# Optimization experiments

Measured on AMD Instinct MI355X. Metric: run time of the kernel, lower is better.

## Reference

```python
import jax, jax.numpy as jnp
import numpy as np

N_STATE, N_CTRL, T, NB = 32, 16, 128, 64
NSC = N_STATE + N_CTRL

mT = lambda m: jnp.swapaxes(m, -1, -2)


def setup_inputs() -> dict:
    key = jax.random.key(0)
    k1, k2, k3, k4, k5, k6 = jax.random.split(key, 6)
    # Q must be PSD (the torch example builds Q = Qr^T Qr); add I for conditioning.
    Qr = jax.random.normal(k1, (NB, T, NSC, NSC), jnp.float32)
    Q = mT(Qr) @ Qr / NSC + jnp.eye(NSC, dtype=jnp.float32)
    p = jax.random.normal(k2, (NB, T, NSC), jnp.float32)
    x_init = jax.random.normal(k3, (NB, N_STATE), jnp.float32)
    # Stable-ish linear dynamics so the T=128 rollout does not blow up.
    A = jnp.tile(0.95 * jnp.eye(N_STATE, dtype=jnp.float32), (NB, 1, 1)) \
        + 0.02 * jax.random.normal(k4, (NB, N_STATE, N_STATE), jnp.float32)
    Bm = 0.1 * jax.random.normal(k5, (NB, N_STATE, N_CTRL), jnp.float32)
    c1 = 0.1 * jax.random.normal(k6, (NB, N_STATE), jnp.float32)
    return {"x_init": x_init, "Q": Q, "p": p, "A": A, "Bm": Bm, "c1": c1}


def _gains(Qt, qt, ns):
    # Qt: [B, nsc, nsc], qt: [B, nsc, 1]
    Qxx, Qxu = Qt[:, :ns, :ns], Qt[:, :ns, ns:]
    Qux, Quu = Qt[:, ns:, :ns], Qt[:, ns:, ns:]
    qx, qu = qt[:, :ns], qt[:, ns:]
    Quu_inv = jnp.linalg.pinv(Quu)          # batched pinv, as in the torch code
    K = -(Quu_inv @ Qux)                    # [B, nc, ns]
    k = -(Quu_inv @ qu)                     # [B, nc, 1]
    KT = mT(K)
    V = Qxx + Qxu @ K + KT @ Qux + KT @ Quu @ K
    v = qx + Qxu @ k + KT @ qu + KT @ Quu @ k
    return K, k, V, v


def _lqr(x_init, Q, p, A, Bm, c1):
    ns = A.shape[-1]
    F = jnp.concatenate([A, Bm], axis=-1)   # [B, ns, nsc]
    FT = mT(F)
    ft = c1[..., None]                       # [B, ns, 1]

    # ---- backward Riccati/DP recursion (sequential over T) ----
    K_last, k_last, V, v = _gains(Q[:, -1], p[:, -1][..., None], ns)

    def bstep(carry, inp):
        Vtp1, vtp1 = carry
        Qt_raw, pt = inp                     # [B,nsc,nsc], [B,nsc]
        Qt = Qt_raw + FT @ Vtp1 @ F
        qt = pt[..., None] + FT @ (Vtp1 @ ft) + FT @ vtp1
        K, k, Vt, vt = _gains(Qt, qt, ns)
        return (Vt, vt), (K, k)

    Qtm = jnp.swapaxes(Q[:, :-1], 0, 1)[::-1]   # [T-1, B, nsc, nsc], t = T-2..0
    ptm = jnp.swapaxes(p[:, :-1], 0, 1)[::-1]
    _, (Ks_rev, ks_rev) = jax.lax.scan(bstep, (V, v), (Qtm, ptm))
    Ks = jnp.concatenate([Ks_rev[::-1], K_last[None]], axis=0)  # [T, B, nc, ns], forward time order
    ks = jnp.concatenate([ks_rev[::-1], k_last[None]], axis=0)  # [T, B, nc, 1]

    # ---- forward rollout ----
    def fstep(x, inp):
        K, k, Qt, pt = inp
        u = jnp.einsum('bij,bj->bi', K, x) + k[..., 0]
        xu = jnp.concatenate([x, u], axis=-1)                 # tau_t, [B, nsc]
        obj = 0.5 * jnp.einsum('bi,bij,bj->b', xu, Qt, xu) + jnp.einsum('bi,bi->b', xu, pt)
        xn = jnp.einsum('bij,bj->bi', A, x) + jnp.einsum('bij,bj->bi', Bm, u) + c1
        return xn, (x, u, obj, xu)

    Qf = jnp.swapaxes(Q, 0, 1)               # [T, B, nsc, nsc]
    pf = jnp.swapaxes(p, 0, 1)
    _, (xs, us, objs, taus) = jax.lax.scan(fstep, x_init, (Ks, ks, Qf, pf))
    # xs: [T, B, ns] (x_0..x_{T-1}, matching torch which does not append x_T)
    return xs, us, objs, taus


def reference(x_init, Q, p, A, Bm, c1):
    return _lqr(x_init, Q, p, A, Bm, c1)
```

## Files before the change

### kernel.cpp

```cpp
#include <hip/hip_runtime.h>

#define TT     128
#define NBATCH 64

#define BAR()  asm volatile("s_waitcnt lgkmcnt(0)\n\ts_barrier" ::: "memory")
#define BARV() asm volatile("s_waitcnt vmcnt(0) lgkmcnt(0)\n\ts_barrier" ::: "memory")

__device__ __forceinline__ void gload16(const float* g, float* l) {
    __builtin_amdgcn_global_load_lds(
        (__attribute__((address_space(1))) void*)g,
        (__attribute__((address_space(3))) void*)l, 16, 0, 0);
}

__device__ __forceinline__ float rdlane(float v, int l) {
    return __int_as_float(__builtin_amdgcn_readlane(__float_as_int(v), l));
}

__device__ __forceinline__ void inv4(const float4 pr[4], float IP[4][4]) {
    float a00=pr[0].x, a01=pr[0].y, a10=pr[1].x, a11=pr[1].y;
    float b00=pr[0].z, b01=pr[0].w, b10=pr[1].z, b11=pr[1].w;
    float c00=pr[2].x, c01=pr[2].y, c10=pr[3].x, c11=pr[3].y;
    float d00=pr[2].z, d01=pr[2].w, d10=pr[3].z, d11=pr[3].w;
    float r = 1.0f / (a00*a11 - a01*a10);
    float ia00 =  a11*r, ia01 = -a01*r, ia10 = -a10*r, ia11 = a00*r;
    float t00 = ia00*b00 + ia01*b10, t01 = ia00*b01 + ia01*b11;
    float t10 = ia10*b00 + ia11*b10, t11 = ia10*b01 + ia11*b11;
    float u00 = c00*ia00 + c01*ia10, u01 = c00*ia01 + c01*ia11;
    float u10 = c10*ia00 + c11*ia10, u11 = c10*ia01 + c11*ia11;
    float s00 = d00 - (c00*t00 + c01*t10), s01 = d01 - (c00*t01 + c01*t11);
    float s10 = d10 - (c10*t00 + c11*t10), s11 = d11 - (c10*t01 + c11*t11);
    float rs = 1.0f / (s00*s11 - s01*s10);
    float is00 =  s11*rs, is01 = -s01*rs, is10 = -s10*rs, is11 = s00*rs;
    float su00 = is00*u00 + is01*u10, su01 = is00*u01 + is01*u11;
    float su10 = is10*u00 + is11*u10, su11 = is10*u01 + is11*u11;
    IP[0][0] = ia00 + (t00*su00 + t01*su10);
    IP[0][1] = ia01 + (t00*su01 + t01*su11);
    IP[1][0] = ia10 + (t10*su00 + t11*su10);
    IP[1][1] = ia11 + (t10*su01 + t11*su11);
    IP[0][2] = -(t00*is00 + t01*is10);  IP[0][3] = -(t00*is01 + t01*is11);
    IP[1][2] = -(t10*is00 + t11*is10);  IP[1][3] = -(t10*is01 + t11*is11);
    IP[2][0] = -su00; IP[2][1] = -su01;
    IP[3][0] = -su10; IP[3][1] = -su11;
    IP[2][2] = is00;  IP[2][3] = is01;
    IP[3][2] = is10;  IP[3][3] = is11;
}

__global__ __launch_bounds__(256, 1)
void lqr_backward(const float* __restrict__ Q, const float* __restrict__ p,
                  const float* __restrict__ A, const float* __restrict__ Bm,
                  const float* __restrict__ c1, float* __restrict__ Kws)
{
    const int b   = blockIdx.x;
    const int tid = threadIdx.x;

    __shared__ __align__(16) float Fs[32*52];
    __shared__ __align__(16) float Vs[32*36];
    __shared__ __align__(16) float Ms[32*52];
    __shared__ __align__(16) float Xs[48*52];
    __shared__ __align__(16) float Qtb[2][48*48];
    __shared__ __align__(16) float qtb[2][256];
    __shared__ __align__(16) float KKs[16*36];
    __shared__ float vsv[32], fts[32], wv[32];

    const int ai0 = (tid / 12) * 4, ac0 = (tid % 12) * 4;
    const int br0 = (tid / 12) * 4, bc0 = (tid % 12) * 4;
    const int pi  = tid >> 3;
    const int pg  = tid & 7;
    const int pj0 = pg * 4;

    for (int st = tid; st < 256; st += 256) {
        int k = st >> 3, q = st & 7;
        ((float4*)(Fs + k*52))[q] = ((const float4*)A)[(b*32 + k)*8 + q];
    }
    for (int st = tid; st < 128; st += 256) {
        int k = st >> 2, q = st & 3;
        ((float4*)(Fs + k*52))[8 + q] = ((const float4*)Bm)[(b*32 + k)*4 + q];
    }
    for (int st = tid; st < 288; st += 256) ((float4*)Vs)[st] = make_float4(0,0,0,0);
    if (tid < 32) { vsv[tid] = 0.0f; fts[tid] = c1[b*32 + tid]; }

    {
        const float* Qs0 = Q + (size_t)(b*TT + TT-1) * 2304;
        #pragma unroll
        for (int r = 0; r < 3; ++r) {
            int e = r*256 + tid;
            if (e < 576) gload16(Qs0 + e*4, Qtb[0] + e*4);
        }
        if (tid < 12) gload16(p + (size_t)(b*TT + TT-1)*48 + tid*4, qtb[0] + tid*4);
    }
    BARV();

    for (int t = TT-1; t >= 0; --t) {
        const int cur = (TT-1 - t) & 1;
        float* Qtc = Qtb[cur];
        float* qtc = qtb[cur];
        float* Kbase = Kws + (size_t)(b*TT + t) * 528;

        if (tid < 96) {
            float4 a0 = make_float4(0,0,0,0), a1 = a0, a2 = a0, a3 = a0;
            #pragma unroll
            for (int k = 0; k < 32; ++k) {
                float4 v = *(const float4*)(Vs + k*36 + ai0);
                float4 f = *(const float4*)(Fs + k*52 + ac0);
                a0.x += v.x*f.x; a0.y += v.x*f.y; a0.z += v.x*f.z; a0.w += v.x*f.w;
                a1.x += v.y*f.x; a1.y += v.y*f.y; a1.z += v.y*f.z; a1.w += v.y*f.w;
                a2.x += v.z*f.x; a2.y += v.z*f.y; a2.z += v.z*f.z; a2.w += v.z*f.w;
                a3.x += v.w*f.x; a3.y += v.w*f.y; a3.z += v.w*f.z; a3.w += v.w*f.w;
            }
            *(float4*)(Ms + (ai0+0)*52 + ac0) = a0;
            *(float4*)(Ms + (ai0+1)*52 + ac0) = a1;
            *(float4*)(Ms + (ai0+2)*52 + ac0) = a2;
            *(float4*)(Ms + (ai0+3)*52 + ac0) = a3;
        } else if (tid >= 192) {
            const int idx = tid - 192;
            if (t > 0) {
                const float* Qs = Q + (size_t)(b*TT + t-1) * 2304;
                float* dst = Qtb[cur ^ 1];
                #pragma unroll
                for (int r = 0; r < 9; ++r) {
                    int e = r*64 + idx;
                    gload16(Qs + e*4, dst + e*4);
                }
                if (idx < 12) gload16(p + (size_t)(b*TT + t-1)*48 + idx*4,
                                      qtb[cur ^ 1] + idx*4);
            }
            if (idx < 32) {
                float acc = vsv[idx];
                #pragma unroll
                for (int k = 0; k < 32; ++k) acc += Vs[idx*36 + k] * fts[k];
                wv[idx] = acc;
            }
        }
        if (tid >= 192) {
            if (t > 0) asm volatile("s_waitcnt vmcnt(10)" ::: "memory");
            else       asm volatile("s_waitcnt vmcnt(0)"  ::: "memory");
        }
        BAR();

        if (tid < 144) {
            float4 a0 = *(const float4*)(Qtc + (br0+0)*48 + bc0);
            float4 a1 = *(const float4*)(Qtc + (br0+1)*48 + bc0);
            float4 a2 = *(const float4*)(Qtc + (br0+2)*48 + bc0);
            float4 a3 = *(const float4*)(Qtc + (br0+3)*48 + bc0);
            #pragma unroll
            for (int k = 0; k < 32; ++k) {
                float4 fr = *(const float4*)(Fs + k*52 + br0);
                float4 mc = *(const float4*)(Ms + k*52 + bc0);
                a0.x += fr.x*mc.x; a0.y += fr.x*mc.y; a0.z += fr.x*mc.z; a0.w += fr.x*mc.w;
                a1.x += fr.y*mc.x; a1.y += fr.y*mc.y; a1.z += fr.y*mc.z; a1.w += fr.y*mc.w;
                a2.x += fr.z*mc.x; a2.y += fr.z*mc.y; a2.z += fr.z*mc.z; a2.w += fr.z*mc.w;
                a3.x += fr.w*mc.x; a3.y += fr.w*mc.y; a3.z += fr.w*mc.z; a3.w += fr.w*mc.w;
            }
            *(float4*)(Xs + (br0+0)*52 + bc0) = a0;
            *(float4*)(Xs + (br0+1)*52 + bc0) = a1;
            *(float4*)(Xs + (br0+2)*52 + bc0) = a2;
            *(float4*)(Xs + (br0+3)*52 + bc0) = a3;
        } else if (tid >= 192 && tid < 240) {
            const int c = tid - 192;
            float acc = qtc[c];
            #pragma unroll
            for (int k = 0; k < 32; ++k) acc += Fs[k*52 + c] * wv[k];
            qtc[c] = acc;
            if (c >= 32) Xs[c*52 + 48] = acc;
        }
        BAR();

        float4 pa0; float pq[16];
        if (tid < 64) {
            const int c = (tid < 49) ? tid : 48;
            float col[16];
            #pragma unroll
            for (int r = 0; r < 16; ++r) col[r] = Xs[(32+r)*52 + c];

            #pragma unroll
            for (int q = 0; q < 4; ++q) {
                const int pc = 32 + 4*q;
                float4 pr[4];
                #pragma unroll
                for (int m = 0; m < 4; ++m) {
                    pr[m].x = rdlane(col[4*q+m], pc+0);
                    pr[m].y = rdlane(col[4*q+m], pc+1);
                    pr[m].z = rdlane(col[4*q+m], pc+2);
                    pr[m].w = rdlane(col[4*q+m], pc+3);
                }
                float IP[4][4];
                inv4(pr, IP);
                float R[4];
                #pragma unroll
                for (int m = 0; m < 4; ++m)
                    R[m] = IP[m][0]*col[4*q+0] + IP[m][1]*col[4*q+1]
                         + IP[m][2]*col[4*q+2] + IP[m][3]*col[4*q+3];
                #pragma unroll
                for (int r = 0; r < 16; ++r) {
                    if ((r >> 2) == q) continue;
                    float f0 = rdlane(col[r], pc+0);
                    float f1 = rdlane(col[r], pc+1);
                    float f2 = rdlane(col[r], pc+2);
                    float f3 = rdlane(col[r], pc+3);
                    col[r] -= f0*R[0] + f1*R[1] + f2*R[2] + f3*R[3];
                }
                #pragma unroll
                for (int m = 0; m < 4; ++m) col[4*q+m] = R[m];
            }

            const int cc = (tid < 32) ? c : 32;
            if (tid < 32 || tid == 48) {
                #pragma unroll
                for (int r = 0; r < 16; ++r) KKs[r*36 + cc] = col[r];
            }
        } else {
            pa0 = *(const float4*)(Xs + pi*52 + pj0);
            #pragma unroll
            for (int m = 0; m < 4; ++m) {
                float4 v4 = *(const float4*)(Xs + pi*52 + 32 + m*4);
                pq[m*4+0] = v4.x; pq[m*4+1] = v4.y;
                pq[m*4+2] = v4.z; pq[m*4+3] = v4.w;
            }
        }
        BAR();

        {
            if (tid < 64) {
                pa0 = *(const float4*)(Xs + pi*52 + pj0);
                #pragma unroll
                for (int m = 0; m < 4; ++m) {
                    float4 v4 = *(const float4*)(Xs + pi*52 + 32 + m*4);
                    pq[m*4+0] = v4.x; pq[m*4+1] = v4.y;
                    pq[m*4+2] = v4.z; pq[m*4+3] = v4.w;
                }
            }
            if (tid < 132) {
                const int ft = tid * 4;
                float4 kv;
                if (ft < 512) {
                    const int c = ft >> 4, r0 = ft & 15;
                    kv.x = -KKs[(r0+0)*36 + c];
                    kv.y = -KKs[(r0+1)*36 + c];
                    kv.z = -KKs[(r0+2)*36 + c];
                    kv.w = -KKs[(r0+3)*36 + c];
                } else {
                    const int r0 = ft - 512;
                    kv.x = -KKs[(r0+0)*36 + 32];
                    kv.y = -KKs[(r0+1)*36 + 32];
                    kv.z = -KKs[(r0+2)*36 + 32];
                    kv.w = -KKs[(r0+3)*36 + 32];
                }
                *(float4*)(Kbase + ft) = kv;
            }
            #pragma unroll
            for (int k = 0; k < 16; ++k) {
                float4 k0 = *(const float4*)(KKs + k*36 + pj0);
                pa0.x -= pq[k]*k0.x; pa0.y -= pq[k]*k0.y;
                pa0.z -= pq[k]*k0.z; pa0.w -= pq[k]*k0.w;
            }
            *(float4*)(Vs + pi*36 + pj0) = pa0;
            if (pg == 0) {
                float accv = qtc[pi];
                #pragma unroll
                for (int k = 0; k < 16; ++k) accv -= pq[k] * KKs[k*36 + 32];
                vsv[pi] = accv;
            }
        }
        BAR();
    }
}

__global__ __launch_bounds__(64, 1)
void lqr_forward(const float* __restrict__ Kws, const float* __restrict__ A,
                 const float* __restrict__ Bm, const float* __restrict__ c1,
                 const float* __restrict__ x_init,
                 float* __restrict__ xs, float* __restrict__ us,
                 float* __restrict__ taus)
{
    const int b = blockIdx.x, l = threadIdx.x;
    __shared__ __align__(16) float Fb[32*48];
    __shared__ __align__(16) float Kb[544];
    __shared__ float c1s[32], xu[48];

    for (int st = l; st < 256; st += 64) {
        int k = st >> 3, q = st & 7;
        ((float4*)Fb)[k*12 + q] = ((const float4*)A)[(b*32 + k)*8 + q];
    }
    for (int st = l; st < 128; st += 64) {
        int k = st >> 2, q = st & 3;
        ((float4*)Fb)[k*12 + 8 + q] = ((const float4*)Bm)[(b*32 + k)*4 + q];
    }
    if (l < 32) { c1s[l] = c1[b*32 + l]; xu[l] = x_init[b*32 + l]; }

    float4 ka, kb, kc = make_float4(0,0,0,0);
    {
        const float4* s0 = (const float4*)(Kws + (size_t)(b*TT) * 528);
        ka = s0[l]; kb = s0[l + 64];
        if (l < 4) kc = s0[l + 128];
    }
    __syncthreads();

    for (int t = 0; t < TT; ++t) {
        ((float4*)Kb)[l]      = ka;
        ((float4*)Kb)[l + 64] = kb;
        if (l < 4) ((float4*)Kb)[l + 128] = kc;
        __syncthreads();

        if (t + 1 < TT) {
            const float4* sn = (const float4*)(Kws + (size_t)(b*TT + t+1) * 528);
            ka = sn[l]; kb = sn[l + 64];
            if (l < 4) kc = sn[l + 128];
        }

        float part = 0.0f;
        int i = l & 15, g = l >> 4;
        #pragma unroll
        for (int jj = 0; jj < 8; ++jj) {
            int j = g*8 + jj;
            part += Kb[j*16 + i] * xu[j];
        }
        part += __shfl_down(part, 32);
        part += __shfl_down(part, 16);
        float ui = part + Kb[512 + i];
        if (l < 16) {
            xu[32 + l] = ui;
            us[(size_t)(t*64 + b)*16 + l] = ui;
        }
        __syncthreads();

        if (l < 32) xs[(size_t)(t*64 + b)*32 + l] = xu[l];
        if (l < 48) taus[(size_t)(t*64 + b)*48 + l] = xu[l];

        float pn = 0.0f;
        int i2 = l & 31, h = l >> 5;
        #pragma unroll
        for (int jj = 0; jj < 24; ++jj) {
            int j = h*24 + jj;
            pn += Fb[i2*48 + j] * xu[j];
        }
        pn += __shfl_down(pn, 32);
        float xni = pn + ((l < 32) ? c1s[i2] : 0.0f);
        __syncthreads();
        if (l < 32) xu[l] = xni;
        __syncthreads();
    }
}

__global__ __launch_bounds__(256, 4)
void lqr_obj(const float* __restrict__ Q, const float* __restrict__ p,
             const float* __restrict__ taus, float* __restrict__ objs)
{
    const int bi = blockIdx.x;
    const int b = bi >> 7, t = bi & 127;
    const int tid = threadIdx.x;
    __shared__ float xu[48];
    __shared__ float red[8];
    const float* tp = taus + (size_t)(t*64 + b)*48;
    if (tid < 48) xu[tid] = tp[tid];
    __syncthreads();

    const float4* Q4 = (const float4*)(Q + (size_t)bi * 2304);
    float acc = 0.0f;
    for (int e4 = tid; e4 < 576; e4 += 256) {
        float4 qv = Q4[e4];
        int r = e4 / 12, c = (e4 % 12) * 4;
        float xr = xu[r];
        acc += xr * (qv.x*xu[c] + qv.y*xu[c+1] + qv.z*xu[c+2] + qv.w*xu[c+3]);
    }
    acc *= 0.5f;
    if (tid < 48) acc += xu[tid] * p[(size_t)bi*48 + tid];

    #pragma unroll
    for (int off = 32; off > 0; off >>= 1) acc += __shfl_down(acc, off);
    if ((tid & 63) == 0) red[tid >> 6] = acc;
    __syncthreads();
    if (tid == 0) objs[(t << 6) + b] = red[0] + red[1] + red[2] + red[3];
}

extern "C" void kernel_launch(void* const* d_in, const int* in_sizes, int n_in,
                              void* d_out, int out_size, void* d_ws, size_t ws_size,
                              hipStream_t stream) {
    const float* x_init = (const float*)d_in[0];
    const float* Q      = (const float*)d_in[1];
    const float* p      = (const float*)d_in[2];
    const float* A      = (const float*)d_in[3];
    const float* Bm     = (const float*)d_in[4];
    const float* c1     = (const float*)d_in[5];

    float* out  = (float*)d_out;
    float* xs   = out;
    float* us   = out + 262144;
    float* objs = out + 393216;
    float* taus = out + 401408;

    float* Kws = (float*)d_ws;

    lqr_backward<<<NBATCH, 256, 0, stream>>>(Q, p, A, Bm, c1, Kws);
    lqr_forward<<<NBATCH, 64, 0, stream>>>(Kws, A, Bm, c1, x_init, xs, us, taus);
    lqr_obj<<<NBATCH*TT, 256, 0, stream>>>(Q, p, taus, objs);
}
```

Measured before the change: 689.0 us.

## Fuse Quu block update into solver wavefront and drop a barrier

After: 714.1 us. 3.6% more time.

```diff
diff --git a/kernel.cpp b/kernel.cpp
--- a/kernel.cpp
+++ b/kernel.cpp
@@ -63,7 +63,9 @@
     __shared__ float vsv[32], fts[32], wv[32];
 
     const int ai0 = (tid / 12) * 4, ac0 = (tid % 12) * 4;
-    const int br0 = (tid / 12) * 4, bc0 = (tid % 12) * 4;
+    const int ur0 = 32 + (tid / 12) * 4, uc0 = ac0;
+    const int xt  = tid - 64;
+    const int xr0 = (xt / 12) * 4, xc0 = (xt % 12) * 4;
     const int pi  = tid >> 3;
     const int pg  = tid & 7;
     const int pj0 = pg * 4;
@@ -137,36 +139,35 @@
         }
         BAR();
 
-        if (tid < 144) {
-            float4 a0 = *(const float4*)(Qtc + (br0+0)*48 + bc0);
-            float4 a1 = *(const float4*)(Qtc + (br0+1)*48 + bc0);
-            float4 a2 = *(const float4*)(Qtc + (br0+2)*48 + bc0);
-            float4 a3 = *(const float4*)(Qtc + (br0+3)*48 + bc0);
-            #pragma unroll
-            for (int k = 0; k < 32; ++k) {
-                float4 fr = *(const float4*)(Fs + k*52 + br0);
-                float4 mc = *(const float4*)(Ms + k*52 + bc0);
-                a0.x += fr.x*mc.x; a0.y += fr.x*mc.y; a0.z += fr.x*mc.z; a0.w += fr.x*mc.w;
-                a1.x += fr.y*mc.x; a1.y += fr.y*mc.y; a1.z += fr.y*mc.z; a1.w += fr.y*mc.w;
-                a2.x += fr.z*mc.x; a2.y += fr.z*mc.y; a2.z += fr.z*mc.z; a2.w += fr.z*mc.w;
-                a3.x += fr.w*mc.x; a3.y += fr.w*mc.y; a3.z += fr.w*mc.z; a3.w += fr.w*mc.w;
-            }
-            *(float4*)(Xs + (br0+0)*52 + bc0) = a0;
-            *(float4*)(Xs + (br0+1)*52 + bc0) = a1;
-            *(float4*)(Xs + (br0+2)*52 + bc0) = a2;
-            *(float4*)(Xs + (br0+3)*52 + bc0) = a3;
-        } else if (tid >= 192 && tid < 240) {
-            const int c = tid - 192;
-            float acc = qtc[c];
-            #pragma unroll
-            for (int k = 0; k < 32; ++k) acc += Fs[k*52 + c] * wv[k];
-            qtc[c] = acc;
-            if (c >= 32) Xs[c*52 + 48] = acc;
-        }
-        BAR();
-
-        float4 pa0; float pq[16];
         if (tid < 64) {
+            if (tid < 48) {
+                float4 a0 = *(const float4*)(Qtc + (ur0+0)*48 + uc0);
+                float4 a1 = *(const float4*)(Qtc + (ur0+1)*48 + uc0);
+                float4 a2 = *(const float4*)(Qtc + (ur0+2)*48 + uc0);
+                float4 a3 = *(const float4*)(Qtc + (ur0+3)*48 + uc0);
+                #pragma unroll
+                for (int k = 0; k < 32; ++k) {
+                    float4 fr = *(const float4*)(Fs + k*52 + ur0);
+                    float4 mc = *(const float4*)(Ms + k*52 + uc0);
+                    a0.x += fr.x*mc.x; a0.y += fr.x*mc.y; a0.z += fr.x*mc.z; a0.w += fr.x*mc.w;
+                    a1.x += fr.y*mc.x; a1.y += fr.y*mc.y; a1.z += fr.y*mc.z; a1.w += fr.y*mc.w;
+                    a2.x += fr.z*mc.x; a2.y += fr.z*mc.y; a2.z += fr.z*mc.z; a2.w += fr.z*mc.w;
+                    a3.x += fr.w*mc.x; a3.y += fr.w*mc.y; a3.z += fr.w*mc.z; a3.w += fr.w*mc.w;
+                }
+                *(float4*)(Xs + (ur0+0)*52 + uc0) = a0;
+                *(float4*)(Xs + (ur0+1)*52 + uc0) = a1;
+                *(float4*)(Xs + (ur0+2)*52 + uc0) = a2;
+                *(float4*)(Xs + (ur0+3)*52 + uc0) = a3;
+            } else {
+                const int i = tid - 48;
+                float acc = qtc[32 + i];
+                #pragma unroll
+                for (int k = 0; k < 32; ++k) acc += Fs[k*52 + 32 + i] * wv[k];
+                Xs[(32 + i)*52 + 48] = acc;
+            }
+            asm volatile("s_waitcnt lgkmcnt(0)" ::: "memory");
+            __builtin_amdgcn_sched_barrier(0);
+
             const int c = (tid < 49) ? tid : 48;
             float col[16];
             #pragma unroll
@@ -208,26 +209,41 @@
                 #pragma unroll
                 for (int r = 0; r < 16; ++r) KKs[r*36 + cc] = col[r];
             }
-        } else {
-            pa0 = *(const float4*)(Xs + pi*52 + pj0);
+        } else if (tid < 160) {
+            float4 a0 = *(const float4*)(Qtc + (xr0+0)*48 + xc0);
+            float4 a1 = *(const float4*)(Qtc + (xr0+1)*48 + xc0);
+            float4 a2 = *(const float4*)(Qtc + (xr0+2)*48 + xc0);
+            float4 a3 = *(const float4*)(Qtc + (xr0+3)*48 + xc0);
+            #pragma unroll
+            for (int k = 0; k < 32; ++k) {
+                float4 fr = *(const float4*)(Fs + k*52 + xr0);
+                float4 mc = *(const float4*)(Ms + k*52 + xc0);
+                a0.x += fr.x*mc.x; a0.y += fr.x*mc.y; a0.z += fr.x*mc.z; a0.w += fr.x*mc.w;
+                a1.x += fr.y*mc.x; a1.y += fr.y*mc.y; a1.z += fr.y*mc.z; a1.w += fr.y*mc.w;
+                a2.x += fr.z*mc.x; a2.y += fr.z*mc.y; a2.z += fr.z*mc.z; a2.w += fr.z*mc.w;
+                a3.x += fr.w*mc.x; a3.y += fr.w*mc.y; a3.z += fr.w*mc.z; a3.w += fr.w*mc.w;
+            }
+            *(float4*)(Xs + (xr0+0)*52 + xc0) = a0;
+            *(float4*)(Xs + (xr0+1)*52 + xc0) = a1;
+            *(float4*)(Xs + (xr0+2)*52 + xc0) = a2;
+            *(float4*)(Xs + (xr0+3)*52 + xc0) = a3;
+        } else if (tid >= 192 && tid < 224) {
+            const int c = tid - 192;
+            float acc = qtc[c];
+            #pragma unroll
+            for (int k = 0; k < 32; ++k) acc += Fs[k*52 + c] * wv[k];
+            qtc[c] = acc;
+        }
+        BAR();
+
+        {
+            float4 pa0 = *(const float4*)(Xs + pi*52 + pj0);
+            float pq[16];
             #pragma unroll
             for (int m = 0; m < 4; ++m) {
                 float4 v4 = *(const float4*)(Xs + pi*52 + 32 + m*4);
                 pq[m*4+0] = v4.x; pq[m*4+1] = v4.y;
                 pq[m*4+2] = v4.z; pq[m*4+3] = v4.w;
-            }
-        }
-        BAR();
-
-        {
-            if (tid < 64) {
-                pa0 = *(const float4*)(Xs + pi*52 + pj0);
-                #pragma unroll
-                for (int m = 0; m < 4; ++m) {
-                    float4 v4 = *(const float4*)(Xs + pi*52 + 32 + m*4);
-                    pq[m*4+0] = v4.x; pq[m*4+1] = v4.y;
-                    pq[m*4+2] = v4.z; pq[m*4+3] = v4.w;
-                }
             }
             if (tid < 132) {
                 const int ft = tid * 4;
```
